# Optimization experiments

Hardware: AMD Instinct MI355X
Metric: run time of the kernel (lower is better)

## Reference

```python
import jax, jax.numpy as jnp
import numpy as np

B, N, S, D, H = 32, 16384, 8, 64, 128  # batch, num_inputs, num_slots, slot_size(==input_size), mlp_hidden
ITERS = 3
EPS = 1e-8
LN_EPS = 1e-5


def _ln(x, g, b):
    m = jnp.mean(x, axis=-1, keepdims=True)
    v = jnp.mean((x - m) ** 2, axis=-1, keepdims=True)
    return (x - m) * jax.lax.rsqrt(v + LN_EPS) * g + b


def setup_inputs() -> dict:
    key = jax.random.key(0)
    ks = jax.random.split(key, 20)
    s = 0.02
    return {
        "x": jax.random.normal(ks[0], (B, N, D), jnp.float32),
        "slot_noise": jax.random.normal(ks[1], (B, S, D), jnp.float32),
        "slots_mu": jax.random.normal(ks[2], (1, S, D), jnp.float32),
        "slots_log_sigma": jax.random.normal(ks[3], (1, S, D), jnp.float32) * 0.1,
        "ln_in_g": jnp.ones((D,), jnp.float32), "ln_in_b": jnp.zeros((D,), jnp.float32),
        "ln_slot_g": jnp.ones((D,), jnp.float32), "ln_slot_b": jnp.zeros((D,), jnp.float32),
        "ln_mlp_g": jnp.ones((D,), jnp.float32), "ln_mlp_b": jnp.zeros((D,), jnp.float32),
        "Wq": jax.random.normal(ks[4], (D, D), jnp.float32) * s,
        "Wk": jax.random.normal(ks[5], (D, D), jnp.float32) * s,
        "Wv": jax.random.normal(ks[6], (D, D), jnp.float32) * s,
        "W_ih": jax.random.normal(ks[7], (3 * D, D), jnp.float32) * s,
        "W_hh": jax.random.normal(ks[8], (3 * D, D), jnp.float32) * s,
        "b_ih": jnp.zeros((3 * D,), jnp.float32),
        "b_hh": jnp.zeros((3 * D,), jnp.float32),
        "W1": jax.random.normal(ks[9], (H, D), jnp.float32) * s,
        "b1": jnp.zeros((H,), jnp.float32),
        "W2": jax.random.normal(ks[10], (D, H), jnp.float32) * s,
        "b2": jnp.zeros((D,), jnp.float32),
    }


def reference(x, slot_noise, slots_mu, slots_log_sigma,
              ln_in_g, ln_in_b, ln_slot_g, ln_slot_b, ln_mlp_g, ln_mlp_b,
              Wq, Wk, Wv, W_ih, W_hh, b_ih, b_hh, W1, b1, W2, b2):
    inputs = _ln(x, ln_in_g, ln_in_b)                      # [B,N,D]
    keys = inputs @ Wk.T                                   # [B,N,D]
    values = inputs @ Wv.T                                 # [B,N,D]
    slots = slots_mu + jnp.exp(slots_log_sigma) * slot_noise  # [B,S,D]
    scale = D ** (-0.5)
    for _ in range(ITERS):
        slots_prev = slots
        q = (_ln(slots, ln_slot_g, ln_slot_b) @ Wq.T) * scale   # [B,S,D]
        attn = jax.nn.softmax(jnp.einsum('bnd,bsd->bns', keys, q), axis=2) + EPS
        attn = attn / jnp.sum(attn, axis=1, keepdims=True)      # weighted mean over inputs
        updates = jnp.einsum('bns,bnd->bsd', attn, values)      # [B,S,D]
        # GRUCell(update, hidden=slots_prev), torch semantics
        gi = updates @ W_ih.T + b_ih
        gh = slots_prev @ W_hh.T + b_hh
        i_r, i_z, i_n = jnp.split(gi, 3, axis=-1)
        h_r, h_z, h_n = jnp.split(gh, 3, axis=-1)
        r = jax.nn.sigmoid(i_r + h_r)
        z = jax.nn.sigmoid(i_z + h_z)
        n = jnp.tanh(i_n + r * h_n)
        upd = (1.0 - z) * n + z * slots_prev
        # residual MLP (full_skip=False: residual around updates)
        slots = upd + jax.nn.relu(_ln(upd, ln_mlp_g, ln_mlp_b) @ W1.T + b1) @ W2.T + b2
    return slots
```

## Files before the change

### kernel.cpp

```cpp
#include <hip/hip_runtime.h>

#define BB 32
#define NN 16384

typedef __attribute__((ext_vector_type(4))) float f4;
typedef __attribute__((ext_vector_type(8))) short short8;

__device__ __forceinline__ unsigned int f2bf(float f) {
  unsigned int u = __float_as_uint(f);
  return (u + 0x7fffu + ((u >> 16) & 1u)) >> 16;
}
__device__ __forceinline__ short bfs(float f) { return (short)f2bf(f); }

__global__ void __launch_bounds__(256) prep_kernel(
    const float* __restrict__ Wq, const float* __restrict__ Wk,
    const float* __restrict__ W_ih, const float* __restrict__ Wv,
    float* __restrict__ M, float* __restrict__ Wihv)
{
  int id = blockIdx.x * 256 + threadIdx.x;
  if (id < 4096) {
    int e1 = id >> 6, e2 = id & 63;
    float acc = 0.f;
    for (int d = 0; d < 64; ++d) acc += Wq[d * 64 + e1] * Wk[d * 64 + e2];
    M[id] = acc;
  } else {
    int t = (id - 4096) >> 6, e = id & 63;
    float acc = 0.f;
    for (int k = 0; k < 64; ++k) acc += W_ih[t * 64 + k] * Wv[k * 64 + e];
    Wihv[t * 64 + e] = acc;
  }
}

__global__ void __launch_bounds__(64) init_qk_kernel(
    const float* __restrict__ noise, const float* __restrict__ mu,
    const float* __restrict__ lsig, float* __restrict__ slots,
    const float* __restrict__ gs, const float* __restrict__ bsl,
    const float* __restrict__ M, unsigned short* __restrict__ qkb)
{
  const int bsi = blockIdx.x, l = threadIdx.x;
  const int idx = bsi * 64 + l;
  __shared__ float sh[64];
  float v = mu[idx & 511] + __expf(lsig[idx & 511]) * noise[idx];
  slots[idx] = v;
  float sm = v, sq = v * v;
#pragma unroll
  for (int m = 1; m < 64; m <<= 1) { sm += __shfl_xor(sm, m); sq += __shfl_xor(sq, m); }
  float mean = sm * (1.f / 64.f);
  float var = sq * (1.f / 64.f) - mean * mean;
  sh[l] = (v - mean) * rsqrtf(var + 1e-5f) * gs[l] + bsl[l];
  float acc = 0.f;
  for (int k = 0; k < 64; ++k) acc += sh[k] * M[k * 64 + l];
  qkb[idx] = (unsigned short)f2bf(acc * 0.125f);
}

template <int MODE>
__global__ void __launch_bounds__(256) attn_kernel(
    const float* __restrict__ x, const unsigned short* __restrict__ Xin,
    const float* __restrict__ gin, const float* __restrict__ bin,
    unsigned short* __restrict__ Xout,
    const unsigned short* __restrict__ qkb,
    float* __restrict__ Wpart, float* __restrict__ cpart)
{
  __shared__ __align__(16) unsigned short XT[4][4608];
  __shared__ __align__(16) unsigned short Pt[4][16][40];
  __shared__ float red[4][512];
  __shared__ float cred[4][8];

  const int tid = threadIdx.x, wave = tid >> 6, lane = tid & 63;
  const int l15 = lane & 15, quad = lane >> 4;
  const int blk = blockIdx.x;
  const int b = blk >> 5;
  const int k0 = quad * 8;

  const unsigned short* qrow = qkb + (((b << 3) + (l15 & 7)) << 6) + k0;
  const short8 qkA0 = *(const short8*)qrow;
  const short8 qkA1 = *(const short8*)(qrow + 32);

  f4 g0a, g0b, g1a, g1b, h0a, h0b, h1a, h1b;
  if constexpr (MODE == 0) {
    g0a = *(const f4*)(gin + k0);      g0b = *(const f4*)(gin + k0 + 4);
    g1a = *(const f4*)(gin + k0 + 32); g1b = *(const f4*)(gin + k0 + 36);
    h0a = *(const f4*)(bin + k0);      h0b = *(const f4*)(bin + k0 + 4);
    h1a = *(const f4*)(bin + k0 + 32); h1b = *(const f4*)(bin + k0 + 36);
  }

  const size_t row00 = (size_t)blk * 512 + wave * 32 + l15;
  unsigned short* xt = &XT[wave][0];

  f4 wacc[4];
#pragma unroll
  for (int t = 0; t < 4; ++t) wacc[t] = (f4){0.f, 0.f, 0.f, 0.f};
  float cacc = 0.f;

  f4 cc[2][4];
  short8 aa[2][2];
  if constexpr (MODE == 0) {
    const float* xp = x + row00 * 64 + k0;
#pragma unroll
    for (int s = 0; s < 2; ++s) {
      const float* sp = xp + s * 1024;
      cc[s][0] = *(const f4*)sp;        cc[s][1] = *(const f4*)(sp + 4);
      cc[s][2] = *(const f4*)(sp + 32); cc[s][3] = *(const f4*)(sp + 36);
    }
  } else {
    const unsigned short* xb = Xin + row00 * 64 + k0;
#pragma unroll
    for (int s = 0; s < 2; ++s) {
      aa[s][0] = *(const short8*)(xb + s * 1024);
      aa[s][1] = *(const short8*)(xb + s * 1024 + 32);
    }
  }

#pragma unroll
  for (int u = 0; u < 4; ++u) {
    f4 nc[2][4];
    short8 na[2][2];
    if (u < 3) {
      if constexpr (MODE == 0) {
        const float* xp = x + (row00 + (size_t)(u + 1) * 128) * 64 + k0;
#pragma unroll
        for (int s = 0; s < 2; ++s) {
          const float* sp = xp + s * 1024;
          nc[s][0] = *(const f4*)sp;        nc[s][1] = *(const f4*)(sp + 4);
          nc[s][2] = *(const f4*)(sp + 32); nc[s][3] = *(const f4*)(sp + 36);
        }
      } else {
        const unsigned short* xb = Xin + (row00 + (size_t)(u + 1) * 128) * 64 + k0;
#pragma unroll
        for (int s = 0; s < 2; ++s) {
          na[s][0] = *(const short8*)(xb + s * 1024);
          na[s][1] = *(const short8*)(xb + s * 1024 + 32);
        }
      }
    }

#pragma unroll
    for (int s = 0; s < 2; ++s) {
      short8 a0, a1;
      if constexpr (MODE == 0) {
        float sm = 0.f, sq = 0.f;
#pragma unroll
        for (int j = 0; j < 4; ++j) {
          float v0 = cc[s][0][j], v1 = cc[s][1][j], v2 = cc[s][2][j], v3 = cc[s][3][j];
          sm += v0 + v1 + v2 + v3;
          sq += v0 * v0 + v1 * v1 + v2 * v2 + v3 * v3;
        }
        sm += __shfl_xor(sm, 16); sq += __shfl_xor(sq, 16);
        sm += __shfl_xor(sm, 32); sq += __shfl_xor(sq, 32);
        const float mean = sm * (1.f / 64.f);
        const float var = sq * (1.f / 64.f) - mean * mean;
        const float rstd = rsqrtf(var + 1e-5f);
#pragma unroll
        for (int j = 0; j < 4; ++j) {
          a0[j]     = bfs((cc[s][0][j] - mean) * rstd * g0a[j] + h0a[j]);
          a0[j + 4] = bfs((cc[s][1][j] - mean) * rstd * g0b[j] + h0b[j]);
          a1[j]     = bfs((cc[s][2][j] - mean) * rstd * g1a[j] + h1a[j]);
          a1[j + 4] = bfs((cc[s][3][j] - mean) * rstd * g1b[j] + h1b[j]);
        }
        unsigned short* xo = Xout + (row00 + (size_t)u * 128 + s * 16) * 64 + k0;
        *(short8*)xo = a0;
        *(short8*)(xo + 32) = a1;
      } else {
        a0 = aa[s][0]; a1 = aa[s][1];
      }

      {
        const int nn = s * 16 + l15;
        unsigned short* xb0 = xt + (quad << 3) + nn;
#pragma unroll
        for (int jj = 0; jj < 8; ++jj) {
          xb0[(k0 + jj) * 72]        = (unsigned short)a0[jj];
          xb0[(k0 + jj + 32) * 72]   = (unsigned short)a1[jj];
        }
      }

      f4 lg = (f4){0.f, 0.f, 0.f, 0.f};
      lg = __builtin_amdgcn_mfma_f32_16x16x32_bf16(a0, qkA0, lg, 0, 0, 0);
      lg = __builtin_amdgcn_mfma_f32_16x16x32_bf16(a1, qkA1, lg, 0, 0, 0);
      float p[4];
#pragma unroll
      for (int r = 0; r < 4; ++r) {
        float e = __expf(lg[r]);
        float ss = e;
        ss += __shfl_xor(ss, 1);
        ss += __shfl_xor(ss, 2);
        ss += __shfl_xor(ss, 4);
        p[r] = e * __builtin_amdgcn_rcpf(ss);
        cacc += p[r];
      }
      unsigned short* pw = &Pt[wave][l15][s * 16 + quad * 4];
      *(unsigned int*)pw = f2bf(p[0]) | (f2bf(p[1]) << 16);
      *(unsigned int*)(pw + 2) = f2bf(p[2]) | (f2bf(p[3]) << 16);
    }

    short8 pf = *(const short8*)&Pt[wave][l15][quad * 8];
#pragma unroll
    for (int t = 0; t < 4; ++t) {
      const int rr = t * 16 + l15;
      const short8 cvv =
          *(const short8*)&xt[rr * 72 + (((rr >> 3) & 3) << 3) + (quad << 3)];
      wacc[t] = __builtin_amdgcn_mfma_f32_16x16x32_bf16(pf, cvv, wacc[t], 0, 0, 0);
    }

    if (u < 3) {
      if constexpr (MODE == 0) {
#pragma unroll
        for (int s = 0; s < 2; ++s)
#pragma unroll
          for (int j = 0; j < 4; ++j) cc[s][j] = nc[s][j];
      } else {
#pragma unroll
        for (int s = 0; s < 2; ++s) { aa[s][0] = na[s][0]; aa[s][1] = na[s][1]; }
      }
    }
  }

  cacc += __shfl_xor(cacc, 16);
  cacc += __shfl_xor(cacc, 32);
  if (lane < 8) cred[wave][lane] = cacc;
  if (quad < 2) {
#pragma unroll
    for (int t = 0; t < 4; ++t)
#pragma unroll
      for (int r = 0; r < 4; ++r)
        red[wave][(quad * 4 + r) * 64 + (t << 4) + l15] = wacc[t][r];
  }
  __syncthreads();
  for (int i = tid; i < 512; i += 256)
    Wpart[(size_t)blk * 512 + i] = red[0][i] + red[1][i] + red[2][i] + red[3][i];
  if (tid < 8)
    cpart[blk * 8 + tid] = cred[0][tid] + cred[1][tid] + cred[2][tid] + cred[3][tid];
}

__global__ void __launch_bounds__(256) update_kernel(
    const float* __restrict__ Wpart, const float* __restrict__ cpart,
    const float* __restrict__ slots, float* __restrict__ out,
    const float* __restrict__ Wihv, const float* __restrict__ W_hh,
    const float* __restrict__ b_ih, const float* __restrict__ b_hh,
    const float* __restrict__ g_mlp, const float* __restrict__ b_mlp,
    const float* __restrict__ W1, const float* __restrict__ b1,
    const float* __restrict__ W2, const float* __restrict__ b2,
    const float* __restrict__ gs, const float* __restrict__ bsl,
    const float* __restrict__ M, unsigned short* __restrict__ qkb, int make_q)
{
  const int bs = blockIdx.x;
  const int b = bs >> 3, s = bs & 7;
  const int tid = threadIdx.x;
  const int l = tid & 63, cq = tid >> 6;
  __shared__ float wred[4][64];
  __shared__ float credS[4];
  __shared__ float u_sh[64], sp_sh[64], giA[192], ghA[192], uln_sh[64], h_sh[128];

  float wp = 0.f, cp2 = 0.f;
  for (int c = cq * 8; c < cq * 8 + 8; ++c) {
    wp += Wpart[(size_t)(((b << 5) + c) * 8 + s) * 64 + l];
    cp2 += cpart[((b << 5) + c) * 8 + s];
  }
  wred[cq][l] = wp;
  if (l == 0) credS[cq] = cp2;
  __syncthreads();

  float sp = 0.f;
  if (tid < 64) {
    const float cs = credS[0] + credS[1] + credS[2] + credS[3];
    const float u = (wred[0][l] + wred[1][l] + wred[2][l] + wred[3][l]) / cs;
    sp = slots[(b * 8 + s) * 64 + l];
    u_sh[l] = u; sp_sh[l] = sp;
  }
  __syncthreads();

  if (tid < 192) {
    float accI = b_ih[tid], accH = b_hh[tid];
    const float* wi = Wihv + tid * 64;
    const float* wh = W_hh + tid * 64;
    for (int k = 0; k < 64; ++k) { accI += u_sh[k] * wi[k]; accH += sp_sh[k] * wh[k]; }
    giA[tid] = accI; ghA[tid] = accH;
  }
  __syncthreads();

  float upd = 0.f;
  if (tid < 64) {
    const float rg = 1.f / (1.f + __expf(-(giA[l] + ghA[l])));
    const float zg = 1.f / (1.f + __expf(-(giA[64 + l] + ghA[64 + l])));
    const float ng = tanhf(giA[128 + l] + rg * ghA[128 + l]);
    upd = (1.f - zg) * ng + zg * sp;
    float sm = upd, sq = upd * upd;
#pragma unroll
    for (int m = 1; m < 64; m <<= 1) { sm += __shfl_xor(sm, m); sq += __shfl_xor(sq, m); }
    const float mean = sm * (1.f / 64.f);
    const float var = sq * (1.f / 64.f) - mean * mean;
    uln_sh[l] = (upd - mean) * rsqrtf(var + 1e-5f) * g_mlp[l] + b_mlp[l];
  }
  __syncthreads();

  if (tid < 128) {
    float acc = b1[tid];
    const float* w1 = W1 + tid * 64;
    for (int k = 0; k < 64; ++k) acc += uln_sh[k] * w1[k];
    h_sh[tid] = fmaxf(acc, 0.f);
  }
  __syncthreads();

  if (tid < 64) {
    float acc = b2[l];
    const float* w2 = W2 + l * 128;
    for (int k = 0; k < 128; ++k) acc += h_sh[k] * w2[k];
    const float sv = upd + acc;
    out[(b * 8 + s) * 64 + l] = sv;
    if (make_q) {
      float sm2 = sv, sq2 = sv * sv;
#pragma unroll
      for (int m = 1; m < 64; m <<= 1) { sm2 += __shfl_xor(sm2, m); sq2 += __shfl_xor(sq2, m); }
      const float mean2 = sm2 * (1.f / 64.f);
      const float var2 = sq2 * (1.f / 64.f) - mean2 * mean2;
      u_sh[l] = (sv - mean2) * rsqrtf(var2 + 1e-5f) * gs[l] + bsl[l];
      float qa = 0.f;
      for (int k = 0; k < 64; ++k) qa += u_sh[k] * M[k * 64 + l];
      qkb[(b * 8 + s) * 64 + l] = (unsigned short)f2bf(qa * 0.125f);
    }
  }
}

extern "C" void kernel_launch(void* const* d_in, const int* in_sizes, int n_in,
                              void* d_out, int out_size, void* d_ws, size_t ws_size,
                              hipStream_t stream) {
  const float* x       = (const float*)d_in[0];
  const float* noise   = (const float*)d_in[1];
  const float* mu      = (const float*)d_in[2];
  const float* lsig    = (const float*)d_in[3];
  const float* ln_in_g = (const float*)d_in[4];
  const float* ln_in_b = (const float*)d_in[5];
  const float* ln_sl_g = (const float*)d_in[6];
  const float* ln_sl_b = (const float*)d_in[7];
  const float* ln_ml_g = (const float*)d_in[8];
  const float* ln_ml_b = (const float*)d_in[9];
  const float* Wq      = (const float*)d_in[10];
  const float* Wk      = (const float*)d_in[11];
  const float* Wv      = (const float*)d_in[12];
  const float* W_ih    = (const float*)d_in[13];
  const float* W_hh    = (const float*)d_in[14];
  const float* b_ih    = (const float*)d_in[15];
  const float* b_hh    = (const float*)d_in[16];
  const float* W1      = (const float*)d_in[17];
  const float* b1      = (const float*)d_in[18];
  const float* W2      = (const float*)d_in[19];
  const float* b2      = (const float*)d_in[20];

  unsigned short* Xn  = (unsigned short*)d_ws;
  unsigned short* qkb = Xn + (size_t)BB * NN * 64;
  float* M     = (float*)(qkb + 16384);
  float* Wihv  = M + 4096;
  float* slots = Wihv + 12288;
  float* Wpart = slots + 16384;
  float* cpart = Wpart + (size_t)1024 * 512;

  prep_kernel<<<dim3(64), dim3(256), 0, stream>>>(Wq, Wk, W_ih, Wv, M, Wihv);
  init_qk_kernel<<<dim3(256), dim3(64), 0, stream>>>(
      noise, mu, lsig, slots, ln_sl_g, ln_sl_b, M, qkb);

  attn_kernel<0><<<dim3(1024), dim3(256), 0, stream>>>(
      x, nullptr, ln_in_g, ln_in_b, Xn, qkb, Wpart, cpart);

  for (int it = 0; it < 3; ++it) {
    update_kernel<<<dim3(256), dim3(256), 0, stream>>>(
        Wpart, cpart, slots, (it == 2) ? (float*)d_out : slots,
        Wihv, W_hh, b_ih, b_hh, ln_ml_g, ln_ml_b, W1, b1, W2, b2,
        ln_sl_g, ln_sl_b, M, qkb, (it < 2) ? 1 : 0);
    if (it < 2)
      attn_kernel<1><<<dim3(1024), dim3(256), 0, stream>>>(
          x, Xn, ln_in_g, ln_in_b, nullptr, qkb, Wpart, cpart);
  }
}
```

Measured before the change: 308.3 us.

## Shrink attention LDS footprint, transpose logits MFMA, and alias reduction buffers

```diff
diff --git a/kernel.cpp b/kernel.cpp
--- a/kernel.cpp
+++ b/kernel.cpp
@@ -61,16 +61,16 @@
     const unsigned short* __restrict__ qkb,
     float* __restrict__ Wpart, float* __restrict__ cpart)
 {
-  __shared__ __align__(16) unsigned short XT[4][4608];
-  __shared__ __align__(16) unsigned short Pt[4][16][40];
-  __shared__ float red[4][512];
-  __shared__ float cred[4][8];
+  __shared__ __align__(16) unsigned short SMEM[16896];
 
   const int tid = threadIdx.x, wave = tid >> 6, lane = tid & 63;
   const int l15 = lane & 15, quad = lane >> 4;
   const int blk = blockIdx.x;
   const int b = blk >> 5;
   const int k0 = quad * 8;
+
+  unsigned short* xt  = SMEM + wave * 3584;
+  unsigned short* Ptw = SMEM + 14336 + wave * 640;
 
   const unsigned short* qrow = qkb + (((b << 3) + (l15 & 7)) << 6) + k0;
   const short8 qkA0 = *(const short8*)qrow;
@@ -85,12 +85,11 @@
   }
 
   const size_t row00 = (size_t)blk * 512 + wave * 32 + l15;
-  unsigned short* xt = &XT[wave][0];
 
   f4 wacc[4];
 #pragma unroll
   for (int t = 0; t < 4; ++t) wacc[t] = (f4){0.f, 0.f, 0.f, 0.f};
-  float cacc = 0.f;
+  float cac0 = 0.f, cac1 = 0.f, cac2 = 0.f, cac3 = 0.f;
 
   f4 cc[2][4];
   short8 aa[2][2];
@@ -169,36 +168,35 @@
         unsigned short* xb0 = xt + (quad << 3) + nn;
 #pragma unroll
         for (int jj = 0; jj < 8; ++jj) {
-          xb0[(k0 + jj) * 72]        = (unsigned short)a0[jj];
-          xb0[(k0 + jj + 32) * 72]   = (unsigned short)a1[jj];
+          xb0[(k0 + jj) * 56]        = (unsigned short)a0[jj];
+          xb0[(k0 + jj + 32) * 56]   = (unsigned short)a1[jj];
         }
       }
 
       f4 lg = (f4){0.f, 0.f, 0.f, 0.f};
-      lg = __builtin_amdgcn_mfma_f32_16x16x32_bf16(a0, qkA0, lg, 0, 0, 0);
-      lg = __builtin_amdgcn_mfma_f32_16x16x32_bf16(a1, qkA1, lg, 0, 0, 0);
-      float p[4];
-#pragma unroll
-      for (int r = 0; r < 4; ++r) {
-        float e = __expf(lg[r]);
-        float ss = e;
-        ss += __shfl_xor(ss, 1);
-        ss += __shfl_xor(ss, 2);
-        ss += __shfl_xor(ss, 4);
-        p[r] = e * __builtin_amdgcn_rcpf(ss);
-        cacc += p[r];
-      }
-      unsigned short* pw = &Pt[wave][l15][s * 16 + quad * 4];
-      *(unsigned int*)pw = f2bf(p[0]) | (f2bf(p[1]) << 16);
-      *(unsigned int*)(pw + 2) = f2bf(p[2]) | (f2bf(p[3]) << 16);
-    }
-
-    short8 pf = *(const short8*)&Pt[wave][l15][quad * 8];
+      lg = __builtin_amdgcn_mfma_f32_16x16x32_bf16(qkA0, a0, lg, 0, 0, 0);
+      lg = __builtin_amdgcn_mfma_f32_16x16x32_bf16(qkA1, a1, lg, 0, 0, 0);
+      const float e0 = __expf(lg[0]), e1 = __expf(lg[1]);
+      const float e2 = __expf(lg[2]), e3 = __expf(lg[3]);
+      float ss = e0 + e1 + e2 + e3;
+      ss += __shfl_xor(ss, 16);
+      ss += __shfl_xor(ss, 32);
+      const float rs = __builtin_amdgcn_rcpf(ss * 0.5f);
+      const float p0 = e0 * rs, p1 = e1 * rs, p2 = e2 * rs, p3 = e3 * rs;
+      cac0 += p0; cac1 += p1; cac2 += p2; cac3 += p3;
+      unsigned short* pw = Ptw + (quad << 2) * 40 + s * 16 + l15;
+      pw[0]   = (unsigned short)f2bf(p0);
+      pw[40]  = (unsigned short)f2bf(p1);
+      pw[80]  = (unsigned short)f2bf(p2);
+      pw[120] = (unsigned short)f2bf(p3);
+    }
+
+    short8 pf = *(const short8*)(Ptw + l15 * 40 + quad * 8);
 #pragma unroll
     for (int t = 0; t < 4; ++t) {
       const int rr = t * 16 + l15;
       const short8 cvv =
-          *(const short8*)&xt[rr * 72 + (((rr >> 3) & 3) << 3) + (quad << 3)];
+          *(const short8*)(xt + rr * 56 + (((rr >> 3) & 3) << 3) + (quad << 3));
       wacc[t] = __builtin_amdgcn_mfma_f32_16x16x32_bf16(pf, cvv, wacc[t], 0, 0, 0);
     }
 
@@ -215,21 +213,37 @@
     }
   }
 
-  cacc += __shfl_xor(cacc, 16);
-  cacc += __shfl_xor(cacc, 32);
-  if (lane < 8) cred[wave][lane] = cacc;
+#pragma unroll
+  for (int m = 1; m < 16; m <<= 1) {
+    cac0 += __shfl_xor(cac0, m); cac1 += __shfl_xor(cac1, m);
+    cac2 += __shfl_xor(cac2, m); cac3 += __shfl_xor(cac3, m);
+  }
+  float* redw  = (float*)(SMEM + wave * 3584);
+  float* credw = (float*)(SMEM + wave * 3584 + 1024);
+  if (l15 == 0 && quad < 2) {
+    credw[quad * 4 + 0] = cac0; credw[quad * 4 + 1] = cac1;
+    credw[quad * 4 + 2] = cac2; credw[quad * 4 + 3] = cac3;
+  }
   if (quad < 2) {
 #pragma unroll
     for (int t = 0; t < 4; ++t)
 #pragma unroll
       for (int r = 0; r < 4; ++r)
-        red[wave][(quad * 4 + r) * 64 + (t << 4) + l15] = wacc[t][r];
-  }
-  __syncthreads();
-  for (int i = tid; i < 512; i += 256)
-    Wpart[(size_t)blk * 512 + i] = red[0][i] + red[1][i] + red[2][i] + red[3][i];
-  if (tid < 8)
-    cpart[blk * 8 + tid] = cred[0][tid] + cred[1][tid] + cred[2][tid] + cred[3][tid];
+        redw[(quad * 4 + r) * 64 + (t << 4) + l15] = wacc[t][r];
+  }
+  __syncthreads();
+  for (int i = tid; i < 512; i += 256) {
+    float acc = 0.f;
+#pragma unroll
+    for (int w = 0; w < 4; ++w) acc += ((const float*)(SMEM + w * 3584))[i];
+    Wpart[(size_t)blk * 512 + i] = acc;
+  }
+  if (tid < 8) {
+    float acc = 0.f;
+#pragma unroll
+    for (int w = 0; w < 4; ++w) acc += ((const float*)(SMEM + w * 3584 + 1024))[tid];
+    cpart[blk * 8 + tid] = acc;
+  }
 }
 
 __global__ void __launch_bounds__(256) update_kernel(
```

Result: faster. 301.3 us (-2.2%).
